# Optimization experiments

Hardware: AMD Instinct MI355X
Metric: run time of the kernel (lower is better)

Reference implementation:

```python
import jax, jax.numpy as jnp
import numpy as np

B, N, DIM = 8, 4096, 512
HEADS, DIM_HEAD = 8, 64
HIDDEN = HEADS * DIM_HEAD
SCALE = DIM_HEAD ** -0.5
NEG = -1e15


def setup_inputs() -> dict:
    key = jax.random.key(0)
    k1, k2, k3, k4, k5 = jax.random.split(key, 5)
    x = jax.random.normal(k1, (B, N, DIM), dtype=jnp.float32)
    lengths = jax.random.randint(k2, (B,), 1, N + 1, dtype=jnp.int64) if jax.config.jax_enable_x64 else jax.random.randint(k2, (B,), 1, N + 1, dtype=jnp.int32)
    w_qkv = jax.random.normal(k3, (3 * HIDDEN, DIM), dtype=jnp.float32) * 0.02
    w_out = jax.random.normal(k4, (DIM, HIDDEN), dtype=jnp.float32) * 0.02
    b_out = jax.random.normal(k5, (DIM,), dtype=jnp.float32) * 0.02
    return {"x": x, "w_qkv": w_qkv, "w_out": w_out, "b_out": b_out, "lengths": lengths}


def reference(x, w_qkv, w_out, b_out, lengths):
    b, n, dim = x.shape
    # positions >= length are masked (equivalent to the cumsum trick in torch)
    pos = jnp.arange(n)
    seq_mask = pos[None, :] >= lengths[:, None]  # (b, n), True => padding

    x = jnp.where(seq_mask[:, :, None], 0.0, x)

    # pointwise Conv1d == matmul over channel dim; channels are head-major
    qkv = jnp.einsum('bnd,ed->bne', x, w_qkv)  # (b, n, 3*hidden)
    q, k, v = jnp.split(qkv, 3, axis=-1)

    def to_heads(t):  # (b, n, hidden) -> (b, heads, dim_head, n)
        return t.reshape(b, n, HEADS, DIM_HEAD).transpose(0, 2, 3, 1)

    q, k, v = to_heads(q), to_heads(k), to_heads(v)
    q = q * SCALE

    m = seq_mask[:, None, None, :]  # (b, 1, 1, n)
    q = jnp.where(m, 0.0, q)
    k = jnp.where(m, NEG, k)
    k = jax.nn.softmax(k, axis=-1)  # softmax over sequence

    context = jnp.einsum('bhdn,bhen->bhde', k, v)   # (b, h, d, d)
    out = jnp.einsum('bhde,bhdn->bhen', context, q)  # (b, h, d, n)
    out = out.transpose(0, 1, 2, 3).reshape(b, HIDDEN, n)  # (b, hidden, n), head-major
    out = jnp.einsum('bcn,dc->bdn', out, w_out) + b_out[None, :, None]
    return out.transpose(0, 2, 1)  # (b, n, dim)
```

## Files before the change

### kernel.cpp

```cpp
#include <hip/hip_runtime.h>

typedef unsigned short u16;
typedef unsigned int u32;
typedef __bf16 bf16x8 __attribute__((ext_vector_type(8)));
typedef float f32x4 __attribute__((ext_vector_type(4)));

#define L2E 1.44269504088896340736f

static __device__ __forceinline__ u16 f2bf(float f) {
  u32 u = __float_as_uint(f);
  u32 r = (u + 0x7fffu + ((u >> 16) & 1u)) >> 16;
  return (u16)r;
}
static __device__ __forceinline__ float bf2f(u32 bits) {
  return __uint_as_float(bits << 16);
}
static __device__ __forceinline__ u32 trunc_bf(float f) {
  return __float_as_uint(f) >> 16;
}

__global__ __launch_bounds__(256) void cvt_x(const float* __restrict__ src,
                                             u16* __restrict__ dst,
                                             const int* __restrict__ lengths) {
  int i = (blockIdx.x * 256 + threadIdx.x) * 8;
  int row = i >> 9;
  if ((row & 4095) >= lengths[row >> 12]) return;
  float4 a = *(const float4*)(src + i);
  float4 b = *(const float4*)(src + i + 4);
  union { u16 h[8]; uint4 v; } o;
  o.h[0] = f2bf(a.x); o.h[1] = f2bf(a.y); o.h[2] = f2bf(a.z); o.h[3] = f2bf(a.w);
  o.h[4] = f2bf(b.x); o.h[5] = f2bf(b.y); o.h[6] = f2bf(b.z); o.h[7] = f2bf(b.w);
  *(uint4*)(dst + i) = o.v;
}

__global__ __launch_bounds__(256) void prep_w(const float* __restrict__ w_qkv,
                                              u16* __restrict__ wqT,
                                              u16* __restrict__ wkvb) {
  __shared__ u16 tile[64][65];
  int bid = blockIdx.x;
  int t = threadIdx.x;
  if (bid < 64) {
    int c0 = (bid & 7) * 64, s0 = (bid >> 3) * 64;
    int r = t >> 4, cc = (t & 15) * 4;
#pragma unroll
    for (int i = 0; i < 4; ++i) {
      int row = r + i * 16;
      float4 v = *(const float4*)(w_qkv + (size_t)(c0 + row) * 512 + s0 + cc);
      tile[row][cc] = f2bf(v.x); tile[row][cc + 1] = f2bf(v.y);
      tile[row][cc + 2] = f2bf(v.z); tile[row][cc + 3] = f2bf(v.w);
    }
    __syncthreads();
#pragma unroll
    for (int i = 0; i < 4; ++i) {
      int srow = r + i * 16;
      union { u16 h[4]; uint2 u; } pk;
#pragma unroll
      for (int j = 0; j < 4; ++j) pk.h[j] = tile[cc + j][srow];
      *(uint2*)(wqT + (size_t)(s0 + srow) * 512 + c0 + cc) = pk.u;
    }
  } else {
    int i = ((bid - 64) * 256 + t) * 8;
    int row = i >> 9, col = i & 511;
    int drow;
    if (row < 512) drow = (row >> 6) * 128 + (row & 63);
    else { int r2 = row - 512; drow = (r2 >> 6) * 128 + 64 + (r2 & 63); }
    const float* src = w_qkv + 262144;
    float4 a = *(const float4*)(src + i);
    float4 b = *(const float4*)(src + i + 4);
    union { u16 h[8]; uint4 v; } o;
    o.h[0] = f2bf(a.x); o.h[1] = f2bf(a.y); o.h[2] = f2bf(a.z); o.h[3] = f2bf(a.w);
    o.h[4] = f2bf(b.x); o.h[5] = f2bf(b.y); o.h[6] = f2bf(b.z); o.h[7] = f2bf(b.w);
    *(uint4*)(wkvb + (size_t)drow * 512 + col) = o.v;
  }
}

__global__ __launch_bounds__(512, 4) void kv_gemm(const u16* __restrict__ A,
                                                  const u16* __restrict__ Bm,
                                                  u16* __restrict__ kvh,
                                                  const int* __restrict__ lengths) {
  __shared__ u16 lA[16384];
  __shared__ u16 lB[8192];

  const int t = threadIdx.x;
  const int w = t >> 6, lane = t & 63, lm = lane & 15, lg = lane >> 4;
  const int wr = w >> 1, wc = w & 1;
  const int h = blockIdx.y;

  int row0, L = 0, myb = -1, panel = 0;
  {
    const int pid = blockIdx.x;
    int pref = 0;
#pragma unroll
    for (int b = 0; b < 8; ++b) {
      int Lb = lengths[b];
      int nb = (Lb + 255) >> 8;
      if (myb < 0 && pid < pref + nb) { myb = b; panel = pid - pref; L = Lb; }
      pref += nb;
    }
    if (myb < 0) return;
    row0 = myb * 4096 + panel * 256;
  }

  const u16* Abase = A + (size_t)row0 * 512;
  const u16* Bbase = Bm + (size_t)h * 128 * 512;

  size_t aoff[4], boff[2];
#pragma unroll
  for (int i = 0; i < 4; ++i) {
    int c = i * 512 + t, r = c >> 3, s = (c & 7) ^ (r & 7);
    aoff[i] = (size_t)r * 512 + s * 8;
  }
#pragma unroll
  for (int i = 0; i < 2; ++i) {
    int c = i * 512 + t, r = c >> 3, s = (c & 7) ^ (r & 7);
    boff[i] = (size_t)r * 512 + s * 8;
  }

  const int swz0 = (lg ^ (lm & 7)) * 8;
  const int swz1 = ((4 + lg) ^ (lm & 7)) * 8;

  f32x4 acc[4][4] = {};

  for (int kt = 0; kt < 8; ++kt) {
    const u16* sa = Abase + kt * 64;
    const u16* sb = Bbase + kt * 64;
#pragma unroll
    for (int i = 0; i < 4; ++i)
      __builtin_amdgcn_global_load_lds(
          (const __attribute__((address_space(1))) void*)(sa + aoff[i]),
          (__attribute__((address_space(3))) void*)(&lA[(i * 512 + w * 64) * 8]),
          16, 0, 0);
#pragma unroll
    for (int i = 0; i < 2; ++i)
      __builtin_amdgcn_global_load_lds(
          (const __attribute__((address_space(1))) void*)(sb + boff[i]),
          (__attribute__((address_space(3))) void*)(&lB[(i * 512 + w * 64) * 8]),
          16, 0, 0);
    __syncthreads();

    const u16* la = &lA[(wr * 64 + lm) * 64];
    const u16* lb = &lB[(wc * 64 + lm) * 64];
    bf16x8 bfr[2][4];
#pragma unroll
    for (int nf = 0; nf < 4; ++nf) {
      bfr[0][nf] = *(const bf16x8*)(lb + nf * 1024 + swz0);
      bfr[1][nf] = *(const bf16x8*)(lb + nf * 1024 + swz1);
    }
#pragma unroll
    for (int mf = 0; mf < 4; ++mf) {
      bf16x8 af0 = *(const bf16x8*)(la + mf * 1024 + swz0);
      bf16x8 af1 = *(const bf16x8*)(la + mf * 1024 + swz1);
      __builtin_amdgcn_s_setprio(1);
#pragma unroll
      for (int nf = 0; nf < 4; ++nf) {
        acc[mf][nf] = __builtin_amdgcn_mfma_f32_16x16x32_bf16(
            bfr[0][nf], af0, acc[mf][nf], 0, 0, 0);
        acc[mf][nf] = __builtin_amdgcn_mfma_f32_16x16x32_bf16(
            bfr[1][nf], af1, acc[mf][nf], 0, 0, 0);
      }
      __builtin_amdgcn_s_setprio(0);
    }
    __syncthreads();
  }

#pragma unroll
  for (int mf = 0; mf < 4; ++mf) {
    int grow = row0 + wr * 64 + mf * 16 + lm;
    int n = grow & 4095;
    bool msk = (n >= L);
    u16* rp = kvh + ((size_t)((myb * 8 + h) * 4096 + n)) * 128 + wc * 64 + lg * 4;
#pragma unroll
    for (int nf = 0; nf < 4; ++nf) {
      int c = wc * 64 + nf * 16 + lg * 4;
      f32x4 v = acc[mf][nf];
      if (msk) {
        float mv = (c < 64) ? -1e15f : 0.f;
        v[0] = mv; v[1] = mv; v[2] = mv; v[3] = mv;
      }
      union { u16 h4[4]; uint2 u; } pk;
      pk.h4[0] = f2bf(v[0]); pk.h4[1] = f2bf(v[1]);
      pk.h4[2] = f2bf(v[2]); pk.h4[3] = f2bf(v[3]);
      *(uint2*)(rp + nf * 16) = pk.u;
    }
  }
}

template <int MODE>
__global__ __launch_bounds__(256, 4) void gemm128(const u16* __restrict__ A,
                                                  const u16* __restrict__ Bm,
                                                  u16* __restrict__ outb,
                                                  float* __restrict__ outf,
                                                  const float* __restrict__ bias,
                                                  const int* __restrict__ lengths) {
  __shared__ u16 lA[8192];
  __shared__ u16 lB[8192];

  const int t = threadIdx.x;
  const int w = t >> 6, lane = t & 63, lm = lane & 15, lg = lane >> 4;
  const int wr = w >> 1, wc = w & 1;
  const int col0 = blockIdx.y * 128;

  int row0, L = 0, myb = -1;
  if constexpr (MODE == 1) {
    row0 = blockIdx.x * 128;
  } else {
    const int pid = blockIdx.x;
    int na[8], pref = 0, panel = 0;
#pragma unroll
    for (int b = 0; b < 8; ++b) {
      int Lb = lengths[b];
      na[b] = (Lb + 127) >> 7;
      if (myb < 0 && pid < pref + na[b]) { myb = b; panel = pid - pref; L = Lb; }
      pref += na[b];
    }
    if (myb < 0) {
      int pid2 = pid - pref, pm = 0;
#pragma unroll
      for (int b = 0; b < 8; ++b) {
        int mb = 32 - na[b];
        if (myb < 0 && pid2 < pm + mb) { myb = b; panel = na[b] + pid2 - pm; }
        pm += mb;
      }
      row0 = myb * 4096 + panel * 128;
      for (int i = t; i < 4096; i += 256) {
        int r = i >> 5, c = (i & 31) * 4;
        *(f32x4*)(outf + (size_t)(row0 + r) * 512 + col0 + c) =
            *(const f32x4*)(bias + col0 + c);
      }
      return;
    }
    row0 = myb * 4096 + panel * 128;
  }

  const u16* Abase = A + (size_t)row0 * 512;
  const u16* Bbase = Bm + (size_t)col0 * 512;
  if constexpr (MODE == 2) Bbase += (size_t)myb * 262144;

  size_t goff[4];
#pragma unroll
  for (int i = 0; i < 4; ++i) {
    int c = i * 256 + t, r = c >> 3, s = (c & 7) ^ (r & 7);
    goff[i] = (size_t)r * 512 + s * 8;
  }

  const int swz0 = (lg ^ (lm & 7)) * 8;
  const int swz1 = ((4 + lg) ^ (lm & 7)) * 8;

  f32x4 acc[4][4] = {};

  for (int kt = 0; kt < 8; ++kt) {
    const u16* sa = Abase + kt * 64;
    const u16* sb = Bbase + kt * 64;
#pragma unroll
    for (int i = 0; i < 4; ++i)
      __builtin_amdgcn_global_load_lds(
          (const __attribute__((address_space(1))) void*)(sa + goff[i]),
          (__attribute__((address_space(3))) void*)(&lA[(i * 256 + w * 64) * 8]),
          16, 0, 0);
#pragma unroll
    for (int i = 0; i < 4; ++i)
      __builtin_amdgcn_global_load_lds(
          (const __attribute__((address_space(1))) void*)(sb + goff[i]),
          (__attribute__((address_space(3))) void*)(&lB[(i * 256 + w * 64) * 8]),
          16, 0, 0);
    __syncthreads();

    const u16* la = &lA[(wr * 64 + lm) * 64];
    const u16* lb = &lB[(wc * 64 + lm) * 64];
    bf16x8 bfr[2][4];
#pragma unroll
    for (int nf = 0; nf < 4; ++nf) {
      bfr[0][nf] = *(const bf16x8*)(lb + nf * 1024 + swz0);
      bfr[1][nf] = *(const bf16x8*)(lb + nf * 1024 + swz1);
    }
#pragma unroll
    for (int mf = 0; mf < 4; ++mf) {
      bf16x8 af0 = *(const bf16x8*)(la + mf * 1024 + swz0);
      bf16x8 af1 = *(const bf16x8*)(la + mf * 1024 + swz1);
      __builtin_amdgcn_s_setprio(1);
#pragma unroll
      for (int nf = 0; nf < 4; ++nf) {
        acc[mf][nf] = __builtin_amdgcn_mfma_f32_16x16x32_bf16(
            bfr[0][nf], af0, acc[mf][nf], 0, 0, 0);
        acc[mf][nf] = __builtin_amdgcn_mfma_f32_16x16x32_bf16(
            bfr[1][nf], af1, acc[mf][nf], 0, 0, 0);
      }
      __builtin_amdgcn_s_setprio(0);
    }
    __syncthreads();
  }

  if constexpr (MODE == 1) {
#pragma unroll
    for (int mf = 0; mf < 4; ++mf) {
      int grow = row0 + wr * 64 + mf * 16 + lm;
      u16* rp = outb + (size_t)grow * 512 + col0 + wc * 64 + lg * 4;
#pragma unroll
      for (int nf = 0; nf < 4; ++nf) {
        f32x4 v = acc[mf][nf];
        union { u16 h4[4]; uint2 u; } pk;
        pk.h4[0] = f2bf(v[0]); pk.h4[1] = f2bf(v[1]);
        pk.h4[2] = f2bf(v[2]); pk.h4[3] = f2bf(v[3]);
        *(uint2*)(rp + nf * 16) = pk.u;
      }
    }
  } else {
    f32x4 b4[4];
#pragma unroll
    for (int nf = 0; nf < 4; ++nf)
      b4[nf] = *(const f32x4*)(bias + col0 + wc * 64 + nf * 16 + lg * 4);
#pragma unroll
    for (int mf = 0; mf < 4; ++mf) {
      int grow = row0 + wr * 64 + mf * 16 + lm;
      bool msk = ((grow & 4095) >= L);
      float* rp = outf + (size_t)grow * 512 + col0 + wc * 64 + lg * 4;
#pragma unroll
      for (int nf = 0; nf < 4; ++nf) {
        f32x4 v = msk ? b4[nf] : (acc[mf][nf] + b4[nf]);
        *(f32x4*)(rp + nf * 16) = v;
      }
    }
  }
}

struct CtxGrp {
  bf16x8 praw[2][2], vraw[2][2];
};

static __device__ __forceinline__ void ctx_load(const u16* __restrict__ base, int g,
                                                int lm, int lg, CtxGrp& X) {
  const u16* rp = base + (size_t)(g * 32 + lm) * 128 + lg * 8;
#pragma unroll
  for (int mt = 0; mt < 2; ++mt)
#pragma unroll
    for (int dh = 0; dh < 2; ++dh) {
      const u16* p = rp + mt * 2048 + dh * 32;
      X.praw[mt][dh] = *(const bf16x8*)(p);
      X.vraw[mt][dh] = *(const bf16x8*)(p + 64);
    }
}

static __device__ __forceinline__ void ctx_compute(const CtxGrp& X, bf16x8 I1, bf16x8 I2,
                                                   f32x4 acc[4][4], float sacc[4]) {
  const f32x4 zero = {0.f, 0.f, 0.f, 0.f};
  bf16x8 pf[2][2];
#pragma unroll
  for (int mt = 0; mt < 2; ++mt)
#pragma unroll
    for (int dh = 0; dh < 2; ++dh) {
      union { bf16x8 v; u32 w4[4]; } in;
      in.v = X.praw[mt][dh];
      union { u16 h[8]; bf16x8 v; } o;
#pragma unroll
      for (int i = 0; i < 4; ++i) {
        float a = bf2f(in.w4[i] & 0xffffu) * L2E;
        float bq = bf2f(in.w4[i] >> 16) * L2E;
        o.h[2 * i] = f2bf(exp2f(a));
        o.h[2 * i + 1] = f2bf(exp2f(bq));
      }
      pf[mt][dh] = o.v;
    }

  f32x4 tP[2][4], tV[2][4];
#pragma unroll
  for (int mt = 0; mt < 2; ++mt)
#pragma unroll
    for (int dh = 0; dh < 2; ++dh) {
      tP[mt][dh * 2] = __builtin_amdgcn_mfma_f32_16x16x32_bf16(pf[mt][dh], I1, zero, 0, 0, 0);
      tP[mt][dh * 2 + 1] = __builtin_amdgcn_mfma_f32_16x16x32_bf16(pf[mt][dh], I2, zero, 0, 0, 0);
      tV[mt][dh * 2] = __builtin_amdgcn_mfma_f32_16x16x32_bf16(X.vraw[mt][dh], I1, zero, 0, 0, 0);
      tV[mt][dh * 2 + 1] = __builtin_amdgcn_mfma_f32_16x16x32_bf16(X.vraw[mt][dh], I2, zero, 0, 0, 0);
    }

#pragma unroll
  for (int dt = 0; dt < 4; ++dt)
#pragma unroll
    for (int mt = 0; mt < 2; ++mt)
      sacc[dt] += tP[mt][dt][0] + tP[mt][dt][1] + tP[mt][dt][2] + tP[mt][dt][3];

  bf16x8 A2[4], B2[4];
#pragma unroll
  for (int dt = 0; dt < 4; ++dt) {
    union { u32 w4[4]; bf16x8 v; } a, bb2;
#pragma unroll
    for (int mt = 0; mt < 2; ++mt) {
      a.w4[mt * 2] = trunc_bf(tP[mt][dt][0]) | (trunc_bf(tP[mt][dt][1]) << 16);
      a.w4[mt * 2 + 1] = trunc_bf(tP[mt][dt][2]) | (trunc_bf(tP[mt][dt][3]) << 16);
      bb2.w4[mt * 2] = trunc_bf(tV[mt][dt][0]) | (trunc_bf(tV[mt][dt][1]) << 16);
      bb2.w4[mt * 2 + 1] = trunc_bf(tV[mt][dt][2]) | (trunc_bf(tV[mt][dt][3]) << 16);
    }
    A2[dt] = a.v; B2[dt] = bb2.v;
  }

#pragma unroll
  for (int dt = 0; dt < 4; ++dt)
#pragma unroll
    for (int et = 0; et < 4; ++et)
      acc[dt][et] = __builtin_amdgcn_mfma_f32_16x16x32_bf16(A2[dt], B2[et], acc[dt][et], 0, 0, 0);
}

__global__ __launch_bounds__(256) void ctx_gemm(const u16* __restrict__ kvh,
                                                float* __restrict__ ctxp,
                                                float* __restrict__ csum,
                                                const int* __restrict__ lengths) {
  int chunk = blockIdx.x;
  int bh = blockIdx.y;
  int b = bh >> 3;
  int L = lengths[b];
  int rows = L - chunk * 512;
  if (rows <= 0) return;

  int t = threadIdx.x;
  int w = t >> 6, lane = t & 63, lm = lane & 15, lg = lane >> 4;

  int wrows = rows - w * 128;
  int ngw = (wrows <= 0) ? 0 : (wrows >= 128 ? 4 : ((wrows + 31) >> 5));

  __shared__ float red[4][4096];
  __shared__ float redc[4][64];

  bf16x8 I1, I2;
  {
    union { u16 h[8]; bf16x8 v; } u1, u2;
#pragma unroll
    for (int j = 0; j < 8; ++j) {
      u1.h[j] = (lg * 8 + j == lm) ? 0x3F80 : 0;
      u2.h[j] = (lg * 8 + j == lm + 16) ? 0x3F80 : 0;
    }
    I1 = u1.v; I2 = u2.v;
  }

  f32x4 acc[4][4] = {};
  float sacc[4] = {};

  const u16* base = kvh + ((size_t)bh * 4096 + (size_t)chunk * 512 + (size_t)w * 128) * 128;

  for (int g = 0; g < ngw; ++g) {
    CtxGrp X;
    ctx_load(base, g, lm, lg, X);
    ctx_compute(X, I1, I2, acc, sacc);
  }

#pragma unroll
  for (int dt = 0; dt < 4; ++dt)
#pragma unroll
    for (int et = 0; et < 4; ++et)
#pragma unroll
      for (int r = 0; r < 4; ++r)
        red[w][(dt * 16 + lg * 4 + r) * 64 + et * 16 + lm] = acc[dt][et][r];
#pragma unroll
  for (int dt = 0; dt < 4; ++dt) {
    float s = sacc[dt];
    s += __shfl_xor(s, 16);
    s += __shfl_xor(s, 32);
    if (lg == 0) redc[w][dt * 16 + lm] = s;
  }
  __syncthreads();

  float* outp = ctxp + ((size_t)bh * 8 + chunk) * 4096;
#pragma unroll
  for (int j = 0; j < 4; ++j) {
    int i = t * 4 + j * 1024;
    f32x4 v = *(const f32x4*)&red[0][i];
    v += *(const f32x4*)&red[1][i];
    v += *(const f32x4*)&red[2][i];
    v += *(const f32x4*)&red[3][i];
    *(f32x4*)(outp + i) = v;
  }
  if (t < 64)
    csum[((size_t)bh * 8 + chunk) * 64 + t] =
        redc[0][t] + redc[1][t] + redc[2][t] + redc[3][t];
}

__global__ __launch_bounds__(256) void reduce_ctx(const float* __restrict__ ctxp,
                                                  float* __restrict__ ctxr,
                                                  const int* __restrict__ lengths) {
  int blk = blockIdx.x;
  int bh = blk >> 2, s = blk & 3;
  int nch = (lengths[bh >> 3] + 511) >> 9;
  int i = s * 1024 + threadIdx.x * 4;
  const float* p = ctxp + (size_t)bh * 8 * 4096 + i;
  f32x4 acc = {0.f, 0.f, 0.f, 0.f};
  for (int ch = 0; ch < nch; ++ch) acc += *(const f32x4*)(p + (size_t)ch * 4096);
  *(f32x4*)(ctxr + (size_t)bh * 4096 + i) = acc;
}

__global__ __launch_bounds__(256) void m_gemm(const float* __restrict__ ctxr,
                                              const float* __restrict__ csum,
                                              const float* __restrict__ w_out,
                                              u16* __restrict__ MT,
                                              const int* __restrict__ lengths) {
  int bh = blockIdx.x;
  int grp = blockIdx.y;
  int b = bh >> 3, h = bh & 7;
  int nch = (lengths[b] + 511) >> 9;
  int dd0 = grp * 128;
  int t = threadIdx.x;
  __shared__ short sctx[64 * 64];
  __shared__ short sw[128 * 64];
  {
    const float* cp = ctxr + (size_t)bh * 4096;
    int i0 = t * 16;
    int d = t >> 2;
    float den = 0.f;
    for (int ch = 0; ch < nch; ++ch) den += csum[((size_t)bh * 8 + ch) * 64 + d];
    float rin = 1.0f / den;
#pragma unroll
    for (int j = 0; j < 16; j += 4) {
      float4 v = *(const float4*)(cp + i0 + j);
      sctx[i0 + j] = (short)f2bf(v.x * rin);
      sctx[i0 + j + 1] = (short)f2bf(v.y * rin);
      sctx[i0 + j + 2] = (short)f2bf(v.z * rin);
      sctx[i0 + j + 3] = (short)f2bf(v.w * rin);
    }
  }
  {
#pragma unroll
    for (int j = 0; j < 32; j += 4) {
      int idx = t * 32 + j;
      int row = idx >> 6, col = idx & 63;
      float4 v = *(const float4*)(w_out + (size_t)(dd0 + row) * 512 + h * 64 + col);
      sw[idx] = (short)f2bf(v.x); sw[idx + 1] = (short)f2bf(v.y);
      sw[idx + 2] = (short)f2bf(v.z); sw[idx + 3] = (short)f2bf(v.w);
    }
  }
  __syncthreads();

  int lane = t & 63, w = t >> 6;
  int lm = lane & 15, lk = (lane >> 4) * 8;
  f32x4 acc[2][4] = {};
#pragma unroll
  for (int kk = 0; kk < 2; ++kk) {
    bf16x8 af[2], bfr[4];
#pragma unroll
    for (int mb = 0; mb < 2; ++mb)
      af[mb] = *(const bf16x8*)(sw + (w * 32 + mb * 16 + lm) * 64 + kk * 32 + lk);
#pragma unroll
    for (int nb = 0; nb < 4; ++nb)
      bfr[nb] = *(const bf16x8*)(sctx + (nb * 16 + lm) * 64 + kk * 32 + lk);
#pragma unroll
    for (int mb = 0; mb < 2; ++mb)
#pragma unroll
      for (int nb = 0; nb < 4; ++nb)
        acc[mb][nb] = __builtin_amdgcn_mfma_f32_16x16x32_bf16(af[mb], bfr[nb], acc[mb][nb], 0, 0, 0);
  }
  u16* outp = MT + (size_t)b * 512 * 512;
#pragma unroll
  for (int mb = 0; mb < 2; ++mb)
#pragma unroll
    for (int r = 0; r < 4; ++r) {
      int dd = dd0 + w * 32 + mb * 16 + (lane >> 4) * 4 + r;
#pragma unroll
      for (int nb = 0; nb < 4; ++nb) {
        int c = h * 64 + nb * 16 + lm;
        outp[dd * 512 + c] = f2bf(acc[mb][nb][r] * 0.125f);
      }
    }
}

extern "C" void kernel_launch(void* const* d_in, const int* in_sizes, int n_in,
                              void* d_out, int out_size, void* d_ws, size_t ws_size,
                              hipStream_t stream) {
  const float* x = (const float*)d_in[0];
  const float* w_qkv = (const float*)d_in[1];
  const float* w_out = (const float*)d_in[2];
  const float* b_out = (const float*)d_in[3];
  const int* lengths = (const int*)d_in[4];
  float* out = (float*)d_out;
  char* ws = (char*)d_ws;

  u16* kvh    = (u16*)(ws);
  u16* xb     = (u16*)(ws + 67108864);
  u16* wkvb   = (u16*)(ws + 100663296);
  u16* wqT    = (u16*)(ws + 101711872);
  float* ctxp = (float*)(ws + 102236160);
  float* csum = (float*)(ws + 110624768);
  float* ctxr = (float*)(ws + 110755840);
  u16* MT     = (u16*)(ws + 111804416);
  u16* G      = (u16*)(ws + 115998720);

  cvt_x<<<8192, 256, 0, stream>>>(x, xb, lengths);
  prep_w<<<320, 256, 0, stream>>>(w_qkv, wqT, wkvb);
  kv_gemm<<<dim3(128, 8), 512, 0, stream>>>(xb, wkvb, kvh, lengths);
  ctx_gemm<<<dim3(8, 64), 256, 0, stream>>>(kvh, ctxp, csum, lengths);
  reduce_ctx<<<256, 256, 0, stream>>>(ctxp, ctxr, lengths);
  m_gemm<<<dim3(64, 4), 256, 0, stream>>>(ctxr, csum, w_out, MT, lengths);
  gemm128<1><<<dim3(32, 4), 256, 0, stream>>>(MT, wqT, G, nullptr, nullptr, nullptr);
  gemm128<2><<<dim3(256, 4), 256, 0, stream>>>(xb, G, nullptr, out, b_out, lengths);
}
```

Measured before the change: 118.4 us.

## Fuse KV projection GEMM with context accumulation via shared-memory tile

Measured after the change: 112.4 us. 5.1% less time.

```diff
diff --git a/kernel.cpp b/kernel.cpp
--- a/kernel.cpp
+++ b/kernel.cpp
@@ -74,12 +74,77 @@
   }
 }
 
-__global__ __launch_bounds__(512, 4) void kv_gemm(const u16* __restrict__ A,
-                                                  const u16* __restrict__ Bm,
-                                                  u16* __restrict__ kvh,
-                                                  const int* __restrict__ lengths) {
-  __shared__ u16 lA[16384];
-  __shared__ u16 lB[8192];
+struct CtxGrp {
+  bf16x8 praw[2][2], vraw[2][2];
+};
+
+static __device__ __forceinline__ void ctx_compute(const CtxGrp& X, bf16x8 I1, bf16x8 I2,
+                                                   f32x4 acc[4][4], float sacc[4]) {
+  const f32x4 zero = {0.f, 0.f, 0.f, 0.f};
+  bf16x8 pf[2][2];
+#pragma unroll
+  for (int mt = 0; mt < 2; ++mt)
+#pragma unroll
+    for (int dh = 0; dh < 2; ++dh) {
+      union { bf16x8 v; u32 w4[4]; } in;
+      in.v = X.praw[mt][dh];
+      union { u16 h[8]; bf16x8 v; } o;
+#pragma unroll
+      for (int i = 0; i < 4; ++i) {
+        float a = bf2f(in.w4[i] & 0xffffu) * L2E;
+        float bq = bf2f(in.w4[i] >> 16) * L2E;
+        o.h[2 * i] = f2bf(exp2f(a));
+        o.h[2 * i + 1] = f2bf(exp2f(bq));
+      }
+      pf[mt][dh] = o.v;
+    }
+
+  f32x4 tP[2][4], tV[2][4];
+#pragma unroll
+  for (int mt = 0; mt < 2; ++mt)
+#pragma unroll
+    for (int dh = 0; dh < 2; ++dh) {
+      tP[mt][dh * 2] = __builtin_amdgcn_mfma_f32_16x16x32_bf16(pf[mt][dh], I1, zero, 0, 0, 0);
+      tP[mt][dh * 2 + 1] = __builtin_amdgcn_mfma_f32_16x16x32_bf16(pf[mt][dh], I2, zero, 0, 0, 0);
+      tV[mt][dh * 2] = __builtin_amdgcn_mfma_f32_16x16x32_bf16(X.vraw[mt][dh], I1, zero, 0, 0, 0);
+      tV[mt][dh * 2 + 1] = __builtin_amdgcn_mfma_f32_16x16x32_bf16(X.vraw[mt][dh], I2, zero, 0, 0, 0);
+    }
+
+#pragma unroll
+  for (int dt = 0; dt < 4; ++dt)
+#pragma unroll
+    for (int mt = 0; mt < 2; ++mt)
+      sacc[dt] += tP[mt][dt][0] + tP[mt][dt][1] + tP[mt][dt][2] + tP[mt][dt][3];
+
+  bf16x8 A2[4], B2[4];
+#pragma unroll
+  for (int dt = 0; dt < 4; ++dt) {
+    union { u32 w4[4]; bf16x8 v; } a, bb2;
+#pragma unroll
+    for (int mt = 0; mt < 2; ++mt) {
+      a.w4[mt * 2] = trunc_bf(tP[mt][dt][0]) | (trunc_bf(tP[mt][dt][1]) << 16);
+      a.w4[mt * 2 + 1] = trunc_bf(tP[mt][dt][2]) | (trunc_bf(tP[mt][dt][3]) << 16);
+      bb2.w4[mt * 2] = trunc_bf(tV[mt][dt][0]) | (trunc_bf(tV[mt][dt][1]) << 16);
+      bb2.w4[mt * 2 + 1] = trunc_bf(tV[mt][dt][2]) | (trunc_bf(tV[mt][dt][3]) << 16);
+    }
+    A2[dt] = a.v; B2[dt] = bb2.v;
+  }
+
+#pragma unroll
+  for (int dt = 0; dt < 4; ++dt)
+#pragma unroll
+    for (int et = 0; et < 4; ++et)
+      acc[dt][et] = __builtin_amdgcn_mfma_f32_16x16x32_bf16(A2[dt], B2[et], acc[dt][et], 0, 0, 0);
+}
+
+__global__ __launch_bounds__(256, 4) void kvctx_gemm(const u16* __restrict__ A,
+                                                     const u16* __restrict__ Bm,
+                                                     float* __restrict__ ctxp,
+                                                     float* __restrict__ csum,
+                                                     const int* __restrict__ lengths) {
+  __shared__ __align__(16) char smem[52224];
+  u16* lA = (u16*)smem;
+  u16* lB = (u16*)(smem + 16384);
 
   const int t = threadIdx.x;
   const int w = t >> 6, lane = t & 63, lm = lane & 15, lg = lane >> 4;
@@ -93,27 +158,22 @@
 #pragma unroll
     for (int b = 0; b < 8; ++b) {
       int Lb = lengths[b];
-      int nb = (Lb + 255) >> 8;
+      int nb = (Lb + 127) >> 7;
       if (myb < 0 && pid < pref + nb) { myb = b; panel = pid - pref; L = Lb; }
       pref += nb;
     }
     if (myb < 0) return;
-    row0 = myb * 4096 + panel * 256;
+    row0 = myb * 4096 + panel * 128;
   }
 
   const u16* Abase = A + (size_t)row0 * 512;
   const u16* Bbase = Bm + (size_t)h * 128 * 512;
 
-  size_t aoff[4], boff[2];
+  size_t goff[4];
 #pragma unroll
   for (int i = 0; i < 4; ++i) {
-    int c = i * 512 + t, r = c >> 3, s = (c & 7) ^ (r & 7);
-    aoff[i] = (size_t)r * 512 + s * 8;
-  }
-#pragma unroll
-  for (int i = 0; i < 2; ++i) {
-    int c = i * 512 + t, r = c >> 3, s = (c & 7) ^ (r & 7);
-    boff[i] = (size_t)r * 512 + s * 8;
+    int c = i * 256 + t, r = c >> 3, s = (c & 7) ^ (r & 7);
+    goff[i] = (size_t)r * 512 + s * 8;
   }
 
   const int swz0 = (lg ^ (lm & 7)) * 8;
@@ -127,19 +187,19 @@
 #pragma unroll
     for (int i = 0; i < 4; ++i)
       __builtin_amdgcn_global_load_lds(
-          (const __attribute__((address_space(1))) void*)(sa + aoff[i]),
-          (__attribute__((address_space(3))) void*)(&lA[(i * 512 + w * 64) * 8]),
+          (const __attribute__((address_space(1))) void*)(sa + goff[i]),
+          (__attribute__((address_space(3))) void*)(lA + (i * 256 + w * 64) * 8),
           16, 0, 0);
 #pragma unroll
-    for (int i = 0; i < 2; ++i)
+    for (int i = 0; i < 4; ++i)
       __builtin_amdgcn_global_load_lds(
-          (const __attribute__((address_space(1))) void*)(sb + boff[i]),
-          (__attribute__((address_space(3))) void*)(&lB[(i * 512 + w * 64) * 8]),
+          (const __attribute__((address_space(1))) void*)(sb + goff[i]),
+          (__attribute__((address_space(3))) void*)(lB + (i * 256 + w * 64) * 8),
           16, 0, 0);
     __syncthreads();
 
-    const u16* la = &lA[(wr * 64 + lm) * 64];
-    const u16* lb = &lB[(wc * 64 + lm) * 64];
+    const u16* la = lA + (wr * 64 + lm) * 64;
+    const u16* lb = lB + (wc * 64 + lm) * 64;
     bf16x8 bfr[2][4];
 #pragma unroll
     for (int nf = 0; nf < 4; ++nf) {
@@ -163,26 +223,90 @@
     __syncthreads();
   }
 
+  u16* tile = (u16*)smem;
 #pragma unroll
   for (int mf = 0; mf < 4; ++mf) {
-    int grow = row0 + wr * 64 + mf * 16 + lm;
-    int n = grow & 4095;
-    bool msk = (n >= L);
-    u16* rp = kvh + ((size_t)((myb * 8 + h) * 4096 + n)) * 128 + wc * 64 + lg * 4;
+    int lrow = wr * 64 + mf * 16 + lm;
+    bool msk = ((panel * 128 + lrow) >= L);
 #pragma unroll
     for (int nf = 0; nf < 4; ++nf) {
-      int c = wc * 64 + nf * 16 + lg * 4;
+      int col = wc * 64 + nf * 16 + lg * 4;
       f32x4 v = acc[mf][nf];
       if (msk) {
-        float mv = (c < 64) ? -1e15f : 0.f;
+        float mv = (col < 64) ? -1e15f : 0.f;
         v[0] = mv; v[1] = mv; v[2] = mv; v[3] = mv;
       }
       union { u16 h4[4]; uint2 u; } pk;
       pk.h4[0] = f2bf(v[0]); pk.h4[1] = f2bf(v[1]);
       pk.h4[2] = f2bf(v[2]); pk.h4[3] = f2bf(v[3]);
-      *(uint2*)(rp + nf * 16) = pk.u;
-    }
-  }
+      *(uint2*)(tile + (size_t)lrow * 136 + col) = pk.u;
+    }
+  }
+  __syncthreads();
+
+  bf16x8 I1, I2;
+  {
+    union { u16 h[8]; bf16x8 v; } u1, u2;
+#pragma unroll
+    for (int j = 0; j < 8; ++j) {
+      u1.h[j] = (lg * 8 + j == lm) ? 0x3F80 : 0;
+      u2.h[j] = (lg * 8 + j == lm + 16) ? 0x3F80 : 0;
+    }
+    I1 = u1.v; I2 = u2.v;
+  }
+  f32x4 acc2[4][4] = {};
+  float sacc[4] = {};
+  {
+    CtxGrp X;
+    const u16* rp = tile + (size_t)(w * 32 + lm) * 136 + lg * 8;
+#pragma unroll
+    for (int mt = 0; mt < 2; ++mt)
+#pragma unroll
+      for (int dh = 0; dh < 2; ++dh) {
+        const u16* p = rp + mt * 16 * 136 + dh * 32;
+        X.praw[mt][dh] = *(const bf16x8*)(p);
+        X.vraw[mt][dh] = *(const bf16x8*)(p + 64);
+      }
+    ctx_compute(X, I1, I2, acc2, sacc);
+  }
+
+  float* red = (float*)(smem + 34816);
+  float* redc = (float*)(smem + 51200);
+
+#pragma unroll
+  for (int dt = 0; dt < 4; ++dt) {
+    float s = sacc[dt];
+    s += __shfl_xor(s, 16);
+    s += __shfl_xor(s, 32);
+    if (lg == 0) redc[w * 64 + dt * 16 + lm] = s;
+  }
+
+#pragma unroll
+  for (int i = 0; i < 4; ++i) {
+    if (w == i) {
+#pragma unroll
+      for (int dt = 0; dt < 4; ++dt)
+#pragma unroll
+        for (int et = 0; et < 4; ++et)
+#pragma unroll
+          for (int r = 0; r < 4; ++r) {
+            int idx = (dt * 16 + lg * 4 + r) * 64 + et * 16 + lm;
+            if (i == 0) red[idx] = acc2[dt][et][r];
+            else red[idx] += acc2[dt][et][r];
+          }
+    }
+    __syncthreads();
+  }
+
+  float* outp = ctxp + ((size_t)((myb * 8 + h) * 32 + panel)) * 4096;
+#pragma unroll
+  for (int j = 0; j < 4; ++j) {
+    int i4 = t * 4 + j * 1024;
+    *(f32x4*)(outp + i4) = *(const f32x4*)(red + i4);
+  }
+  if (t < 64)
+    csum[((size_t)((myb * 8 + h) * 32 + panel)) * 64 + t] =
+        redc[t] + redc[64 + t] + redc[128 + t] + redc[192 + t];
 }
 
 template <int MODE>
@@ -323,163 +447,14 @@
   }
 }
 
-struct CtxGrp {
-  bf16x8 praw[2][2], vraw[2][2];
-};
-
-static __device__ __forceinline__ void ctx_load(const u16* __restrict__ base, int g,
-                                                int lm, int lg, CtxGrp& X) {
-  const u16* rp = base + (size_t)(g * 32 + lm) * 128 + lg * 8;
-#pragma unroll
-  for (int mt = 0; mt < 2; ++mt)
-#pragma unroll
-    for (int dh = 0; dh < 2; ++dh) {
-      const u16* p = rp + mt * 2048 + dh * 32;
-      X.praw[mt][dh] = *(const bf16x8*)(p);
-      X.vraw[mt][dh] = *(const bf16x8*)(p + 64);
-    }
-}
-
-static __device__ __forceinline__ void ctx_compute(const CtxGrp& X, bf16x8 I1, bf16x8 I2,
-                                                   f32x4 acc[4][4], float sacc[4]) {
-  const f32x4 zero = {0.f, 0.f, 0.f, 0.f};
-  bf16x8 pf[2][2];
-#pragma unroll
-  for (int mt = 0; mt < 2; ++mt)
-#pragma unroll
-    for (int dh = 0; dh < 2; ++dh) {
-      union { bf16x8 v; u32 w4[4]; } in;
-      in.v = X.praw[mt][dh];
-      union { u16 h[8]; bf16x8 v; } o;
-#pragma unroll
-      for (int i = 0; i < 4; ++i) {
-        float a = bf2f(in.w4[i] & 0xffffu) * L2E;
-        float bq = bf2f(in.w4[i] >> 16) * L2E;
-        o.h[2 * i] = f2bf(exp2f(a));
-        o.h[2 * i + 1] = f2bf(exp2f(bq));
-      }
-      pf[mt][dh] = o.v;
-    }
-
-  f32x4 tP[2][4], tV[2][4];
-#pragma unroll
-  for (int mt = 0; mt < 2; ++mt)
-#pragma unroll
-    for (int dh = 0; dh < 2; ++dh) {
-      tP[mt][dh * 2] = __builtin_amdgcn_mfma_f32_16x16x32_bf16(pf[mt][dh], I1, zero, 0, 0, 0);
-      tP[mt][dh * 2 + 1] = __builtin_amdgcn_mfma_f32_16x16x32_bf16(pf[mt][dh], I2, zero, 0, 0, 0);
-      tV[mt][dh * 2] = __builtin_amdgcn_mfma_f32_16x16x32_bf16(X.vraw[mt][dh], I1, zero, 0, 0, 0);
-      tV[mt][dh * 2 + 1] = __builtin_amdgcn_mfma_f32_16x16x32_bf16(X.vraw[mt][dh], I2, zero, 0, 0, 0);
-    }
-
-#pragma unroll
-  for (int dt = 0; dt < 4; ++dt)
-#pragma unroll
-    for (int mt = 0; mt < 2; ++mt)
-      sacc[dt] += tP[mt][dt][0] + tP[mt][dt][1] + tP[mt][dt][2] + tP[mt][dt][3];
-
-  bf16x8 A2[4], B2[4];
-#pragma unroll
-  for (int dt = 0; dt < 4; ++dt) {
-    union { u32 w4[4]; bf16x8 v; } a, bb2;
-#pragma unroll
-    for (int mt = 0; mt < 2; ++mt) {
-      a.w4[mt * 2] = trunc_bf(tP[mt][dt][0]) | (trunc_bf(tP[mt][dt][1]) << 16);
-      a.w4[mt * 2 + 1] = trunc_bf(tP[mt][dt][2]) | (trunc_bf(tP[mt][dt][3]) << 16);
-      bb2.w4[mt * 2] = trunc_bf(tV[mt][dt][0]) | (trunc_bf(tV[mt][dt][1]) << 16);
-      bb2.w4[mt * 2 + 1] = trunc_bf(tV[mt][dt][2]) | (trunc_bf(tV[mt][dt][3]) << 16);
-    }
-    A2[dt] = a.v; B2[dt] = bb2.v;
-  }
-
-#pragma unroll
-  for (int dt = 0; dt < 4; ++dt)
-#pragma unroll
-    for (int et = 0; et < 4; ++et)
-      acc[dt][et] = __builtin_amdgcn_mfma_f32_16x16x32_bf16(A2[dt], B2[et], acc[dt][et], 0, 0, 0);
-}
-
-__global__ __launch_bounds__(256) void ctx_gemm(const u16* __restrict__ kvh,
-                                                float* __restrict__ ctxp,
-                                                float* __restrict__ csum,
-                                                const int* __restrict__ lengths) {
-  int chunk = blockIdx.x;
-  int bh = blockIdx.y;
-  int b = bh >> 3;
-  int L = lengths[b];
-  int rows = L - chunk * 512;
-  if (rows <= 0) return;
-
-  int t = threadIdx.x;
-  int w = t >> 6, lane = t & 63, lm = lane & 15, lg = lane >> 4;
-
-  int wrows = rows - w * 128;
-  int ngw = (wrows <= 0) ? 0 : (wrows >= 128 ? 4 : ((wrows + 31) >> 5));
-
-  __shared__ float red[4][4096];
-  __shared__ float redc[4][64];
-
-  bf16x8 I1, I2;
-  {
-    union { u16 h[8]; bf16x8 v; } u1, u2;
-#pragma unroll
-    for (int j = 0; j < 8; ++j) {
-      u1.h[j] = (lg * 8 + j == lm) ? 0x3F80 : 0;
-      u2.h[j] = (lg * 8 + j == lm + 16) ? 0x3F80 : 0;
-    }
-    I1 = u1.v; I2 = u2.v;
-  }
-
-  f32x4 acc[4][4] = {};
-  float sacc[4] = {};
-
-  const u16* base = kvh + ((size_t)bh * 4096 + (size_t)chunk * 512 + (size_t)w * 128) * 128;
-
-  for (int g = 0; g < ngw; ++g) {
-    CtxGrp X;
-    ctx_load(base, g, lm, lg, X);
-    ctx_compute(X, I1, I2, acc, sacc);
-  }
-
-#pragma unroll
-  for (int dt = 0; dt < 4; ++dt)
-#pragma unroll
-    for (int et = 0; et < 4; ++et)
-#pragma unroll
-      for (int r = 0; r < 4; ++r)
-        red[w][(dt * 16 + lg * 4 + r) * 64 + et * 16 + lm] = acc[dt][et][r];
-#pragma unroll
-  for (int dt = 0; dt < 4; ++dt) {
-    float s = sacc[dt];
-    s += __shfl_xor(s, 16);
-    s += __shfl_xor(s, 32);
-    if (lg == 0) redc[w][dt * 16 + lm] = s;
-  }
-  __syncthreads();
-
-  float* outp = ctxp + ((size_t)bh * 8 + chunk) * 4096;
-#pragma unroll
-  for (int j = 0; j < 4; ++j) {
-    int i = t * 4 + j * 1024;
-    f32x4 v = *(const f32x4*)&red[0][i];
-    v += *(const f32x4*)&red[1][i];
-    v += *(const f32x4*)&red[2][i];
-    v += *(const f32x4*)&red[3][i];
-    *(f32x4*)(outp + i) = v;
-  }
-  if (t < 64)
-    csum[((size_t)bh * 8 + chunk) * 64 + t] =
-        redc[0][t] + redc[1][t] + redc[2][t] + redc[3][t];
-}
-
 __global__ __launch_bounds__(256) void reduce_ctx(const float* __restrict__ ctxp,
                                                   float* __restrict__ ctxr,
                                                   const int* __restrict__ lengths) {
   int blk = blockIdx.x;
   int bh = blk >> 2, s = blk & 3;
-  int nch = (lengths[bh >> 3] + 511) >> 9;
+  int nch = (lengths[bh >> 3] + 127) >> 7;
   int i = s * 1024 + threadIdx.x * 4;
-  const float* p = ctxp + (size_t)bh * 8 * 4096 + i;
+  const float* p = ctxp + (size_t)bh * 32 * 4096 + i;
   f32x4 acc = {0.f, 0.f, 0.f, 0.f};
   for (int ch = 0; ch < nch; ++ch) acc += *(const f32x4*)(p + (size_t)ch * 4096);
   *(f32x4*)(ctxr + (size_t)bh * 4096 + i) = acc;
@@ -493,7 +468,7 @@
   int bh = blockIdx.x;
   int grp = blockIdx.y;
   int b = bh >> 3, h = bh & 7;
-  int nch = (lengths[b] + 511) >> 9;
+  int nch = (lengths[b] + 127) >> 7;
   int dd0 = grp * 128;
   int t = threadIdx.x;
   __shared__ short sctx[64 * 64];
@@ -503,7 +478,7 @@
     int i0 = t * 16;
     int d = t >> 2;
     float den = 0.f;
-    for (int ch = 0; ch < nch; ++ch) den += csum[((size_t)bh * 8 + ch) * 64 + d];
+    for (int ch = 0; ch < nch; ++ch) den += csum[((size_t)bh * 32 + ch) * 64 + d];
     float rin = 1.0f / den;
 #pragma unroll
     for (int j = 0; j < 16; j += 4) {
@@ -569,20 +544,18 @@
   float* out = (float*)d_out;
   char* ws = (char*)d_ws;
 
-  u16* kvh    = (u16*)(ws);
-  u16* xb     = (u16*)(ws + 67108864);
-  u16* wkvb   = (u16*)(ws + 100663296);
-  u16* wqT    = (u16*)(ws + 101711872);
-  float* ctxp = (float*)(ws + 102236160);
-  float* csum = (float*)(ws + 110624768);
-  float* ctxr = (float*)(ws + 110755840);
-  u16* MT     = (u16*)(ws + 111804416);
-  u16* G      = (u16*)(ws + 115998720);
+  u16* xb     = (u16*)(ws);
+  u16* wkvb   = (u16*)(ws + 33554432);
+  u16* wqT    = (u16*)(ws + 34603008);
+  float* ctxp = (float*)(ws + 35127296);
+  float* csum = (float*)(ws + 68681728);
+  float* ctxr = (float*)(ws + 69206016);
+  u16* MT     = (u16*)(ws + 70254592);
+  u16* G      = (u16*)(ws + 74448896);
 
   cvt_x<<<8192, 256, 0, stream>>>(x, xb, lengths);
   prep_w<<<320, 256, 0, stream>>>(w_qkv, wqT, wkvb);
-  kv_gemm<<<dim3(128, 8), 512, 0, stream>>>(xb, wkvb, kvh, lengths);
-  ctx_gemm<<<dim3(8, 64), 256, 0, stream>>>(kvh, ctxp, csum, lengths);
+  kvctx_gemm<<<dim3(256, 8), 256, 0, stream>>>(xb, wkvb, ctxp, csum, lengths);
   reduce_ctx<<<256, 256, 0, stream>>>(ctxp, ctxr, lengths);
   m_gemm<<<dim3(64, 4), 256, 0, stream>>>(ctxr, csum, w_out, MT, lengths);
   gemm128<1><<<dim3(32, 4), 256, 0, stream>>>(MT, wqT, G, nullptr, nullptr, nullptr);
```
